# Optimization experiments

Measured on AMD Instinct MI355X. Metric: run time of the kernel, lower is better.

## Reference

```python
import jax, jax.numpy as jnp
import numpy as np

EMB = 1024
HID = 1024

def setup_inputs() -> dict:
    key = jax.random.key(0)
    ks = jax.random.split(key, 7)
    x = jax.random.normal(ks[0], (4, 2048, EMB), dtype=jnp.float32)
    s = 1.0 / np.sqrt(EMB)
    Wq = jax.random.normal(ks[1], (EMB, HID), dtype=jnp.float32) * s
    bq = jnp.zeros((HID,), dtype=jnp.float32)
    Wk = jax.random.normal(ks[2], (EMB, HID), dtype=jnp.float32) * s
    bk = jnp.zeros((HID,), dtype=jnp.float32)
    Wv = jax.random.normal(ks[3], (EMB, HID), dtype=jnp.float32) * s
    bv = jnp.zeros((HID,), dtype=jnp.float32)
    return {"x": x, "Wq": Wq, "bq": bq, "Wk": Wk, "bk": bk, "Wv": Wv, "bv": bv}

def reference(x, Wq, bq, Wk, bk, Wv, bv):
    # x: [B, S, E]
    B, S, _ = x.shape
    Q = x @ Wq + bq  # [B, S, H]
    K = x @ Wk + bk
    V = x @ Wv + bv
    scale = 1.0 / jnp.sqrt(jnp.asarray(Wq.shape[1], dtype=x.dtype))
    scores = jnp.einsum('bqh,bkh->bqk', Q, K) * scale  # [B, S, S]
    causal = jnp.tril(jnp.ones((S, S), dtype=bool))
    scores = jnp.where(causal, scores, -jnp.inf)
    weights = jax.nn.softmax(scores, axis=-1)
    return jnp.einsum('bqk,bkh->bqh', weights, V)
```

## Files before the change

kernel.cpp:

```cpp
#include <hip/hip_runtime.h>
#include <hip/hip_bf16.h>

typedef __attribute__((ext_vector_type(8))) short bf16x8;
typedef __attribute__((ext_vector_type(4))) float f32x4;
typedef __attribute__((ext_vector_type(4))) unsigned short us4;

#define B_ 4
#define S_ 2048
#define E_ 1024
#define H_ 1024
#define M_ (B_ * S_)
#define N3_ (3 * H_)
#define NTRI_ 136

__device__ __forceinline__ unsigned short f2bf(float f) {
  union { float f; unsigned u; } v; v.f = f;
  unsigned r = v.u + 0x7fffu + ((v.u >> 16) & 1u);
  return (unsigned short)(r >> 16);
}
__device__ __forceinline__ float bf2f(unsigned short u) {
  union { unsigned u; float f; } v; v.u = ((unsigned)u) << 16; return v.f;
}

__global__ __launch_bounds__(256) void k_convert_x(const float* __restrict__ x,
                                                   unsigned short* __restrict__ xb) {
  int i = blockIdx.x * 256 + threadIdx.x;
  const float4 v = reinterpret_cast<const float4*>(x)[i];
  us4 o;
  o[0] = f2bf(v.x); o[1] = f2bf(v.y); o[2] = f2bf(v.z); o[3] = f2bf(v.w);
  reinterpret_cast<us4*>(xb)[i] = o;
}

__global__ __launch_bounds__(256) void k_transpose_w(const float* __restrict__ Wq,
                                                     const float* __restrict__ Wk,
                                                     const float* __restrict__ Wv,
                                                     unsigned short* __restrict__ Wt) {
  __shared__ float tile[32][33];
  const int mat = blockIdx.z;
  const float* W = (mat == 0) ? Wq : (mat == 1) ? Wk : Wv;
  const int n0 = blockIdx.x * 32, k0 = blockIdx.y * 32;
  const int tx = threadIdx.x, ty = threadIdx.y;
#pragma unroll
  for (int i = 0; i < 32; i += 8)
    tile[ty + i][tx] = W[(size_t)(k0 + ty + i) * H_ + n0 + tx];
  __syncthreads();
#pragma unroll
  for (int i = 0; i < 32; i += 8) {
    int n = n0 + ty + i;
    Wt[(size_t)(mat * H_ + n) * E_ + k0 + tx] = f2bf(tile[tx][ty + i]);
  }
}

__global__ __launch_bounds__(256, 2) void k_gemm_qkv(
    const unsigned short* __restrict__ xb, const unsigned short* __restrict__ Wt,
    const float* __restrict__ bq, const float* __restrict__ bk,
    const float* __restrict__ bv,
    unsigned short* __restrict__ Qb, unsigned short* __restrict__ Kb,
    unsigned short* __restrict__ Vt) {
  __shared__ unsigned short As[128 * 64];
  __shared__ unsigned short Bs[128 * 64];
  const int nwg = gridDim.x;
  const int cpx = nwg >> 3;
  int bid = blockIdx.x;
  bid = (bid & 7) * cpx + (bid >> 3);
  const int tm = bid / 24, tn = bid % 24;
  const int gm = tm * 128, gn = tn * 128;
  const int tid = threadIdx.x, w = tid >> 6, lane = tid & 63;
  const int wr = w >> 1, wc = w & 1;
  const int srow = lane >> 3;
  const int schunk = (lane & 7) ^ srow;

  f32x4 acc[4][4];
#pragma unroll
  for (int i = 0; i < 4; ++i)
#pragma unroll
    for (int j = 0; j < 4; ++j) acc[i][j] = (f32x4)0.0f;

  for (int kt = 0; kt < 16; ++kt) {
    const int k0 = kt * 64;
#pragma unroll
    for (int i = 0; i < 4; ++i) {
      const int row = w * 32 + i * 8 + srow;
      __builtin_amdgcn_global_load_lds(
          (const __attribute__((address_space(1))) unsigned int*)(xb + (size_t)(gm + row) * E_ + k0 + schunk * 8),
          (__attribute__((address_space(3))) unsigned int*)(As + (w * 32 + i * 8) * 64),
          16, 0, 0);
    }
#pragma unroll
    for (int i = 0; i < 4; ++i) {
      const int row = w * 32 + i * 8 + srow;
      __builtin_amdgcn_global_load_lds(
          (const __attribute__((address_space(1))) unsigned int*)(Wt + (size_t)(gn + row) * E_ + k0 + schunk * 8),
          (__attribute__((address_space(3))) unsigned int*)(Bs + (w * 32 + i * 8) * 64),
          16, 0, 0);
    }
    __syncthreads();
#pragma unroll
    for (int ks = 0; ks < 2; ++ks) {
      bf16x8 af[4], bfrag[4];
#pragma unroll
      for (int mt = 0; mt < 4; ++mt) {
        const int r16 = wr * 64 + mt * 16 + (lane & 15);
        const int ch = (ks * 4 + (lane >> 4)) ^ (r16 & 7);
        af[mt] = *reinterpret_cast<const bf16x8*>(&As[r16 * 64 + ch * 8]);
      }
#pragma unroll
      for (int nt = 0; nt < 4; ++nt) {
        const int c16 = wc * 64 + nt * 16 + (lane & 15);
        const int ch = (ks * 4 + (lane >> 4)) ^ (c16 & 7);
        bfrag[nt] = *reinterpret_cast<const bf16x8*>(&Bs[c16 * 64 + ch * 8]);
      }
#pragma unroll
      for (int mt = 0; mt < 4; ++mt)
#pragma unroll
        for (int nt = 0; nt < 4; ++nt)
          acc[mt][nt] = __builtin_amdgcn_mfma_f32_16x16x32_bf16(
              af[mt], bfrag[nt], acc[mt][nt], 0, 0, 0);
    }
    __syncthreads();
  }

  const int matid = gn >> 10;
  const float* bias = (matid == 0) ? bq : (matid == 1) ? bk : bv;
#pragma unroll
  for (int mt = 0; mt < 4; ++mt) {
#pragma unroll
    for (int nt = 0; nt < 4; ++nt) {
      const int row0 = gm + wr * 64 + mt * 16 + (lane >> 4) * 4;
      const int col = gn + wc * 64 + nt * 16 + (lane & 15);
      const int h = col & 1023;
      const float bb = bias[h];
      if (matid < 2) {
        unsigned short* dst = matid ? Kb : Qb;
#pragma unroll
        for (int r = 0; r < 4; ++r)
          dst[(size_t)(row0 + r) * H_ + h] = f2bf(acc[mt][nt][r] + bb);
      } else {
        const int bat = row0 >> 11, s0 = row0 & 2047;
        us4 pk;
#pragma unroll
        for (int r = 0; r < 4; ++r) pk[r] = f2bf(acc[mt][nt][r] + bb);
        *reinterpret_cast<us4*>(&Vt[(size_t)bat * H_ * S_ + (size_t)h * S_ + s0]) = pk;
      }
    }
  }
}

__global__ __launch_bounds__(256, 2) void k_gemm_scores(
    const unsigned short* __restrict__ Qb, const unsigned short* __restrict__ Kb,
    unsigned short* __restrict__ Pt) {
  __shared__ unsigned short As[128 * 64];
  __shared__ unsigned short Bs[128 * 64];
  int bid = blockIdx.x;
  bid = (bid & 7) * 68 + (bid >> 3);
  const int batch = bid / NTRI_;
  const int t = bid % NTRI_;
  int tm = 0;
  while ((tm + 1) * (tm + 2) / 2 <= t) ++tm;
  const int tn = t - tm * (tm + 1) / 2;
  const int gm = tm * 128, gn = tn * 128;
  const int tid = threadIdx.x, w = tid >> 6, lane = tid & 63;
  const int wr = w >> 1, wc = w & 1;
  const int srow = lane >> 3;
  const int schunk = (lane & 7) ^ srow;
  const unsigned short* Abase = Qb + (size_t)batch * S_ * H_;
  const unsigned short* Bbase = Kb + (size_t)batch * S_ * H_;

  f32x4 acc[4][4];
#pragma unroll
  for (int i = 0; i < 4; ++i)
#pragma unroll
    for (int j = 0; j < 4; ++j) acc[i][j] = (f32x4)0.0f;

  for (int kt = 0; kt < 16; ++kt) {
    const int k0 = kt * 64;
#pragma unroll
    for (int i = 0; i < 4; ++i) {
      const int row = w * 32 + i * 8 + srow;
      __builtin_amdgcn_global_load_lds(
          (const __attribute__((address_space(1))) unsigned int*)(Abase + (size_t)(gm + row) * H_ + k0 + schunk * 8),
          (__attribute__((address_space(3))) unsigned int*)(As + (w * 32 + i * 8) * 64),
          16, 0, 0);
      __builtin_amdgcn_global_load_lds(
          (const __attribute__((address_space(1))) unsigned int*)(Bbase + (size_t)(gn + row) * H_ + k0 + schunk * 8),
          (__attribute__((address_space(3))) unsigned int*)(Bs + (w * 32 + i * 8) * 64),
          16, 0, 0);
    }
    __syncthreads();
#pragma unroll
    for (int ks = 0; ks < 2; ++ks) {
      bf16x8 af[4], bfrag[4];
#pragma unroll
      for (int mt = 0; mt < 4; ++mt) {
        const int r16 = wr * 64 + mt * 16 + (lane & 15);
        const int ch = (ks * 4 + (lane >> 4)) ^ (r16 & 7);
        af[mt] = *reinterpret_cast<const bf16x8*>(&As[r16 * 64 + ch * 8]);
      }
#pragma unroll
      for (int nt = 0; nt < 4; ++nt) {
        const int c16 = wc * 64 + nt * 16 + (lane & 15);
        const int ch = (ks * 4 + (lane >> 4)) ^ (c16 & 7);
        bfrag[nt] = *reinterpret_cast<const bf16x8*>(&Bs[c16 * 64 + ch * 8]);
      }
#pragma unroll
      for (int mt = 0; mt < 4; ++mt)
#pragma unroll
        for (int nt = 0; nt < 4; ++nt)
          acc[mt][nt] = __builtin_amdgcn_mfma_f32_16x16x32_bf16(
              af[mt], bfrag[nt], acc[mt][nt], 0, 0, 0);
    }
    __syncthreads();
  }

  const size_t tbase = ((size_t)batch * NTRI_ + (tm * (tm + 1)) / 2 + tn) * 16384;
#pragma unroll
  for (int mt = 0; mt < 4; ++mt) {
#pragma unroll
    for (int nt = 0; nt < 4; ++nt) {
      const int row0 = wr * 64 + mt * 16 + (lane >> 4) * 4;
      const int col = wc * 64 + nt * 16 + (lane & 15);
#pragma unroll
      for (int r = 0; r < 4; ++r)
        Pt[tbase + (size_t)(row0 + r) * 128 + col] = f2bf(acc[mt][nt][r] * 0.03125f);
    }
  }
}

__global__ __launch_bounds__(256) void k_softmax(unsigned short* __restrict__ Pt) {
  const int tid = threadIdx.x, lane = tid & 63;
  const int gr = blockIdx.x * 4 + (tid >> 6);
  const int batch = gr >> 11, q = gr & 2047;
  const int tm = q >> 7, r = q & 127;
  const int W = (tm + 1) << 7;
  const size_t rowb = ((size_t)batch * NTRI_ + (tm * (tm + 1)) / 2) * 16384 + (size_t)r * 128;

  float s[32];
  float mx = -1e30f;
#pragma unroll
  for (int it = 0; it < 4; ++it) {
    const int c = it * 512 + lane * 8;
    if (c < W) {
      const int tn = c >> 7;
      const bf16x8 v = *reinterpret_cast<const bf16x8*>(&Pt[rowb + (size_t)tn * 16384 + (c & 127)]);
#pragma unroll
      for (int j = 0; j < 8; ++j) {
        float f = bf2f((unsigned short)v[j]);
        if (c + j > q) f = -1e30f;
        s[it * 8 + j] = f;
        mx = fmaxf(mx, f);
      }
    } else {
#pragma unroll
      for (int j = 0; j < 8; ++j) s[it * 8 + j] = -1e30f;
    }
  }
#pragma unroll
  for (int off = 32; off; off >>= 1) mx = fmaxf(mx, __shfl_xor(mx, off));
  float sum = 0.f;
#pragma unroll
  for (int it = 0; it < 4; ++it)
#pragma unroll
    for (int j = 0; j < 8; ++j) {
      const float p = __expf(s[it * 8 + j] - mx);
      s[it * 8 + j] = p;
      sum += p;
    }
#pragma unroll
  for (int off = 32; off; off >>= 1) sum += __shfl_xor(sum, off);
  const float inv = 1.0f / sum;
#pragma unroll
  for (int it = 0; it < 4; ++it) {
    const int c = it * 512 + lane * 8;
    if (c < W) {
      const int tn = c >> 7;
      bf16x8 o;
#pragma unroll
      for (int j = 0; j < 8; ++j) o[j] = (short)f2bf(s[it * 8 + j] * inv);
      *reinterpret_cast<bf16x8*>(&Pt[rowb + (size_t)tn * 16384 + (c & 127)]) = o;
    }
  }
}

__global__ __launch_bounds__(256, 2) void k_gemm_pv(
    const unsigned short* __restrict__ Pt, const unsigned short* __restrict__ Vt,
    float* __restrict__ out) {
  __shared__ unsigned short As[128 * 64];
  __shared__ unsigned short Bs[128 * 64];
  const int b0 = blockIdx.x;
  const int rk = (b0 < 256) ? b0 : 767 - b0;
  const int tm = 15 - (rk >> 5);
  const int batch = (rk >> 3) & 3;
  const int tn = rk & 7;
  const int gm = tm * 128, gn = tn * 128;
  const int tid = threadIdx.x, w = tid >> 6, lane = tid & 63;
  const int wr = w >> 1, wc = w & 1;
  const int srow = lane >> 3;
  const int schunk = (lane & 7) ^ srow;
  const size_t trow = ((size_t)batch * NTRI_ + (tm * (tm + 1)) / 2) * 16384;
  const unsigned short* Bbase = Vt + (size_t)batch * H_ * S_;
  const int nk = (tm + 1) * 2;

  f32x4 acc[4][4];
#pragma unroll
  for (int i = 0; i < 4; ++i)
#pragma unroll
    for (int j = 0; j < 4; ++j) acc[i][j] = (f32x4)0.0f;

  for (int kt = 0; kt < nk; ++kt) {
    const int ktn = kt >> 1, cin = (kt & 1) * 64;
#pragma unroll
    for (int i = 0; i < 4; ++i) {
      const int row = w * 32 + i * 8 + srow;
      __builtin_amdgcn_global_load_lds(
          (const __attribute__((address_space(1))) unsigned int*)(Pt + trow + (size_t)ktn * 16384 + (size_t)row * 128 + cin + schunk * 8),
          (__attribute__((address_space(3))) unsigned int*)(As + (w * 32 + i * 8) * 64),
          16, 0, 0);
      __builtin_amdgcn_global_load_lds(
          (const __attribute__((address_space(1))) unsigned int*)(Bbase + (size_t)(gn + row) * S_ + kt * 64 + schunk * 8),
          (__attribute__((address_space(3))) unsigned int*)(Bs + (w * 32 + i * 8) * 64),
          16, 0, 0);
    }
    __syncthreads();
#pragma unroll
    for (int ks = 0; ks < 2; ++ks) {
      bf16x8 af[4], bfrag[4];
#pragma unroll
      for (int mt = 0; mt < 4; ++mt) {
        const int r16 = wr * 64 + mt * 16 + (lane & 15);
        const int ch = (ks * 4 + (lane >> 4)) ^ (r16 & 7);
        af[mt] = *reinterpret_cast<const bf16x8*>(&As[r16 * 64 + ch * 8]);
      }
#pragma unroll
      for (int nt = 0; nt < 4; ++nt) {
        const int c16 = wc * 64 + nt * 16 + (lane & 15);
        const int ch = (ks * 4 + (lane >> 4)) ^ (c16 & 7);
        bfrag[nt] = *reinterpret_cast<const bf16x8*>(&Bs[c16 * 64 + ch * 8]);
      }
#pragma unroll
      for (int mt = 0; mt < 4; ++mt)
#pragma unroll
        for (int nt = 0; nt < 4; ++nt)
          acc[mt][nt] = __builtin_amdgcn_mfma_f32_16x16x32_bf16(
              af[mt], bfrag[nt], acc[mt][nt], 0, 0, 0);
    }
    __syncthreads();
  }

#pragma unroll
  for (int mt = 0; mt < 4; ++mt) {
#pragma unroll
    for (int nt = 0; nt < 4; ++nt) {
      const int row0 = gm + wr * 64 + mt * 16 + (lane >> 4) * 4;
      const int col = gn + wc * 64 + nt * 16 + (lane & 15);
#pragma unroll
      for (int r = 0; r < 4; ++r)
        out[(size_t)batch * S_ * H_ + (size_t)(row0 + r) * H_ + col] = acc[mt][nt][r];
    }
  }
}

extern "C" void kernel_launch(void* const* d_in, const int* in_sizes, int n_in,
                              void* d_out, int out_size, void* d_ws, size_t ws_size,
                              hipStream_t stream) {
  const float* x  = (const float*)d_in[0];
  const float* Wq = (const float*)d_in[1];
  const float* bq = (const float*)d_in[2];
  const float* Wk = (const float*)d_in[3];
  const float* bk = (const float*)d_in[4];
  const float* Wv = (const float*)d_in[5];
  const float* bv = (const float*)d_in[6];
  float* out = (float*)d_out;

  unsigned short* Qb = (unsigned short*)d_ws;
  unsigned short* Kb = Qb + (size_t)M_ * H_;
  unsigned short* Vt = Kb + (size_t)M_ * H_;
  unsigned short* Xr = Vt + (size_t)M_ * H_;
  unsigned short* xb = Xr;
  unsigned short* Wt = Xr + (size_t)M_ * E_;
  unsigned short* Pt = Xr;

  hipLaunchKernelGGL(k_convert_x, dim3(M_ * E_ / 1024), dim3(256), 0, stream, x, xb);
  hipLaunchKernelGGL(k_transpose_w, dim3(32, 32, 3), dim3(32, 8), 0, stream, Wq, Wk, Wv, Wt);
  hipLaunchKernelGGL(k_gemm_qkv, dim3(1536), dim3(256), 0, stream,
                     xb, Wt, bq, bk, bv, Qb, Kb, Vt);
  hipLaunchKernelGGL(k_gemm_scores, dim3(544), dim3(256), 0, stream, Qb, Kb, Pt);
  hipLaunchKernelGGL(k_softmax, dim3(2048), dim3(256), 0, stream, Pt);
  hipLaunchKernelGGL(k_gemm_pv, dim3(512), dim3(256), 0, stream, Pt, Vt, out);
}
```

Before: 152.5 us.

## Fuse softmax into score GEMM epilogue and defer normalization to PV

Drops the separate softmax pass. The score GEMM epilogue now applies exp directly, without subtracting a row max, zeroes masked entries, writes unnormalized probabilities and atomically accumulates row sums. The PV GEMM divides its output by those sums. This removes a full read-modify-write of the probability buffer and one launch. The x-convert and weight-transpose kernels are also merged into one launch. Skipping the max subtraction risks overflow for large scores, and the change adds atomics and a memset.

```diff
diff --git a/kernel.cpp b/kernel.cpp
--- a/kernel.cpp
+++ b/kernel.cpp
@@ -12,41 +12,41 @@
 #define M_ (B_ * S_)
 #define N3_ (3 * H_)
 #define NTRI_ 136
+#define NCONV_ (M_ * E_ / 1024)
 
 __device__ __forceinline__ unsigned short f2bf(float f) {
   union { float f; unsigned u; } v; v.f = f;
   unsigned r = v.u + 0x7fffu + ((v.u >> 16) & 1u);
   return (unsigned short)(r >> 16);
 }
-__device__ __forceinline__ float bf2f(unsigned short u) {
-  union { unsigned u; float f; } v; v.u = ((unsigned)u) << 16; return v.f;
-}
-
-__global__ __launch_bounds__(256) void k_convert_x(const float* __restrict__ x,
-                                                   unsigned short* __restrict__ xb) {
-  int i = blockIdx.x * 256 + threadIdx.x;
-  const float4 v = reinterpret_cast<const float4*>(x)[i];
-  us4 o;
-  o[0] = f2bf(v.x); o[1] = f2bf(v.y); o[2] = f2bf(v.z); o[3] = f2bf(v.w);
-  reinterpret_cast<us4*>(xb)[i] = o;
-}
-
-__global__ __launch_bounds__(256) void k_transpose_w(const float* __restrict__ Wq,
-                                                     const float* __restrict__ Wk,
-                                                     const float* __restrict__ Wv,
-                                                     unsigned short* __restrict__ Wt) {
+
+__global__ __launch_bounds__(256) void k_prep(
+    const float* __restrict__ x, const float* __restrict__ Wq,
+    const float* __restrict__ Wk, const float* __restrict__ Wv,
+    unsigned short* __restrict__ xb, unsigned short* __restrict__ Wt) {
   __shared__ float tile[32][33];
-  const int mat = blockIdx.z;
+  const int b = blockIdx.x;
+  if (b < NCONV_) {
+    const int i = b * 256 + threadIdx.x;
+    const float4 v = reinterpret_cast<const float4*>(x)[i];
+    us4 o;
+    o[0] = f2bf(v.x); o[1] = f2bf(v.y); o[2] = f2bf(v.z); o[3] = f2bf(v.w);
+    reinterpret_cast<us4*>(xb)[i] = o;
+    return;
+  }
+  const int bb = b - NCONV_;
+  const int mat = bb >> 10;
+  const int rem = bb & 1023;
+  const int n0 = (rem & 31) * 32, k0 = (rem >> 5) * 32;
   const float* W = (mat == 0) ? Wq : (mat == 1) ? Wk : Wv;
-  const int n0 = blockIdx.x * 32, k0 = blockIdx.y * 32;
-  const int tx = threadIdx.x, ty = threadIdx.y;
+  const int tx = threadIdx.x & 31, ty = threadIdx.x >> 5;
 #pragma unroll
   for (int i = 0; i < 32; i += 8)
     tile[ty + i][tx] = W[(size_t)(k0 + ty + i) * H_ + n0 + tx];
   __syncthreads();
 #pragma unroll
   for (int i = 0; i < 32; i += 8) {
-    int n = n0 + ty + i;
+    const int n = n0 + ty + i;
     Wt[(size_t)(mat * H_ + n) * E_ + k0 + tx] = f2bf(tile[tx][ty + i]);
   }
 }
@@ -148,7 +148,7 @@
 
 __global__ __launch_bounds__(256, 2) void k_gemm_scores(
     const unsigned short* __restrict__ Qb, const unsigned short* __restrict__ Kb,
-    unsigned short* __restrict__ Pt) {
+    unsigned short* __restrict__ Pt, float* __restrict__ Sums) {
   __shared__ unsigned short As[128 * 64];
   __shared__ unsigned short Bs[128 * 64];
   int bid = blockIdx.x;
@@ -213,77 +213,37 @@
   }
 
   const size_t tbase = ((size_t)batch * NTRI_ + (tm * (tm + 1)) / 2 + tn) * 16384;
+  const int hi4 = (lane >> 4) * 4, l15 = lane & 15;
 #pragma unroll
   for (int mt = 0; mt < 4; ++mt) {
+    const int row0 = wr * 64 + mt * 16 + hi4;
+    float rsum[4] = {0.f, 0.f, 0.f, 0.f};
 #pragma unroll
     for (int nt = 0; nt < 4; ++nt) {
-      const int row0 = wr * 64 + mt * 16 + (lane >> 4) * 4;
-      const int col = wc * 64 + nt * 16 + (lane & 15);
+      const int col = wc * 64 + nt * 16 + l15;
+#pragma unroll
+      for (int r = 0; r < 4; ++r) {
+        float p = (gn + col > gm + row0 + r) ? 0.0f
+                                             : __expf(acc[mt][nt][r] * 0.03125f);
+        Pt[tbase + (size_t)(row0 + r) * 128 + col] = f2bf(p);
+        rsum[r] += p;
+      }
+    }
+#pragma unroll
+    for (int r = 0; r < 4; ++r)
+#pragma unroll
+      for (int off = 8; off; off >>= 1) rsum[r] += __shfl_xor(rsum[r], off);
+    if (l15 == 0) {
 #pragma unroll
       for (int r = 0; r < 4; ++r)
-        Pt[tbase + (size_t)(row0 + r) * 128 + col] = f2bf(acc[mt][nt][r] * 0.03125f);
-    }
-  }
-}
-
-__global__ __launch_bounds__(256) void k_softmax(unsigned short* __restrict__ Pt) {
-  const int tid = threadIdx.x, lane = tid & 63;
-  const int gr = blockIdx.x * 4 + (tid >> 6);
-  const int batch = gr >> 11, q = gr & 2047;
-  const int tm = q >> 7, r = q & 127;
-  const int W = (tm + 1) << 7;
-  const size_t rowb = ((size_t)batch * NTRI_ + (tm * (tm + 1)) / 2) * 16384 + (size_t)r * 128;
-
-  float s[32];
-  float mx = -1e30f;
-#pragma unroll
-  for (int it = 0; it < 4; ++it) {
-    const int c = it * 512 + lane * 8;
-    if (c < W) {
-      const int tn = c >> 7;
-      const bf16x8 v = *reinterpret_cast<const bf16x8*>(&Pt[rowb + (size_t)tn * 16384 + (c & 127)]);
-#pragma unroll
-      for (int j = 0; j < 8; ++j) {
-        float f = bf2f((unsigned short)v[j]);
-        if (c + j > q) f = -1e30f;
-        s[it * 8 + j] = f;
-        mx = fmaxf(mx, f);
-      }
-    } else {
-#pragma unroll
-      for (int j = 0; j < 8; ++j) s[it * 8 + j] = -1e30f;
-    }
-  }
-#pragma unroll
-  for (int off = 32; off; off >>= 1) mx = fmaxf(mx, __shfl_xor(mx, off));
-  float sum = 0.f;
-#pragma unroll
-  for (int it = 0; it < 4; ++it)
-#pragma unroll
-    for (int j = 0; j < 8; ++j) {
-      const float p = __expf(s[it * 8 + j] - mx);
-      s[it * 8 + j] = p;
-      sum += p;
-    }
-#pragma unroll
-  for (int off = 32; off; off >>= 1) sum += __shfl_xor(sum, off);
-  const float inv = 1.0f / sum;
-#pragma unroll
-  for (int it = 0; it < 4; ++it) {
-    const int c = it * 512 + lane * 8;
-    if (c < W) {
-      const int tn = c >> 7;
-      bf16x8 o;
-#pragma unroll
-      for (int j = 0; j < 8; ++j) o[j] = (short)f2bf(s[it * 8 + j] * inv);
-      *reinterpret_cast<bf16x8*>(&Pt[rowb + (size_t)tn * 16384 + (c & 127)]) = o;
+        atomicAdd(&Sums[batch * S_ + gm + row0 + r], rsum[r]);
     }
   }
 }
 
 __global__ __launch_bounds__(256, 2) void k_gemm_pv(
     const unsigned short* __restrict__ Pt, const unsigned short* __restrict__ Vt,
-    float* __restrict__ out) {
+    const float* __restrict__ Sums, float* __restrict__ out) {
   __shared__ unsigned short As[128 * 64];
   __shared__ unsigned short Bs[128 * 64];
   const int b0 = blockIdx.x;
@@ -348,13 +308,15 @@
 
 #pragma unroll
   for (int mt = 0; mt < 4; ++mt) {
+    const int row0 = gm + wr * 64 + mt * 16 + (lane >> 4) * 4;
+    const f32x4 sv = *reinterpret_cast<const f32x4*>(&Sums[batch * S_ + row0]);
 #pragma unroll
     for (int nt = 0; nt < 4; ++nt) {
-      const int row0 = gm + wr * 64 + mt * 16 + (lane >> 4) * 4;
       const int col = gn + wc * 64 + nt * 16 + (lane & 15);
 #pragma unroll
       for (int r = 0; r < 4; ++r)
-        out[(size_t)batch * S_ * H_ + (size_t)(row0 + r) * H_ + col] = acc[mt][nt][r];
+        out[(size_t)batch * S_ * H_ + (size_t)(row0 + r) * H_ + col] =
+            acc[mt][nt][r] / sv[r];
     }
   }
 }
@@ -378,12 +340,13 @@
   unsigned short* xb = Xr;
   unsigned short* Wt = Xr + (size_t)M_ * E_;
   unsigned short* Pt = Xr;
-
-  hipLaunchKernelGGL(k_convert_x, dim3(M_ * E_ / 1024), dim3(256), 0, stream, x, xb);
-  hipLaunchKernelGGL(k_transpose_w, dim3(32, 32, 3), dim3(32, 8), 0, stream, Wq, Wk, Wv, Wt);
+  float* Sums = (float*)(Xr + 9437184);
+
+  hipLaunchKernelGGL(k_prep, dim3(NCONV_ + 3072), dim3(256), 0, stream,
+                     x, Wq, Wk, Wv, xb, Wt);
   hipLaunchKernelGGL(k_gemm_qkv, dim3(1536), dim3(256), 0, stream,
                      xb, Wt, bq, bk, bv, Qb, Kb, Vt);
-  hipLaunchKernelGGL(k_gemm_scores, dim3(544), dim3(256), 0, stream, Qb, Kb, Pt);
-  hipLaunchKernelGGL(k_softmax, dim3(2048), dim3(256), 0, stream, Pt);
-  hipLaunchKernelGGL(k_gemm_pv, dim3(512), dim3(256), 0, stream, Pt, Vt, out);
-}
+  hipMemsetAsync(Sums, 0, M_ * sizeof(float), stream);
+  hipLaunchKernelGGL(k_gemm_scores, dim3(544), dim3(256), 0, stream, Qb, Kb, Pt, Sums);
+  hipLaunchKernelGGL(k_gemm_pv, dim3(512), dim3(256), 0, stream, Pt, Vt, Sums, out);
+}
```

Result: faster. 147.0 us (-3.6%).
